# Optimization experiments

Measured on AMD Instinct MI355X. Metric: run time of the kernel, lower is better.

## Reference

```python
import jax, jax.numpy as jnp
import numpy as np

N = 20000   # nodes
E = 320000  # edges
C = 64      # channel multiplicity
NB = 8      # bessel basis size
NA = 4      # node attribute (species) dim
L_DIMS = (1, 3, 5)  # 2l+1 for l=0,1,2
SH = 9      # total spherical-harmonic dim
OFFS = (0, 1, 4, 9)


def setup_inputs() -> dict:
    key = jax.random.key(0)
    ks = jax.random.split(key, 11)
    s = lambda k, shape: jax.random.normal(k, shape, dtype=jnp.float32)
    return {
        "length": jax.random.uniform(ks[0], (E, NB), dtype=jnp.float32),
        "node_features": s(ks[1], (N, C)),
        "node_attributes": s(ks[2], (N, NA)),
        "edge_attributes": s(ks[3], (E, SH)),
        "W1": s(ks[4], (NB, 64)),
        "W2": s(ks[5], (64, 64)),
        "W3": s(ks[6], (64, 64)),
        "W4": s(ks[7], (64, 3 * C)),
        "Wl": s(ks[8], (3, C, C)),
        "Wsc": s(ks[9], (NA, C, C)),
        "edge_index": jax.random.randint(ks[10], (2, E), 0, N, dtype=jnp.int32),
    }


def reference(length, node_features, node_attributes, edge_attributes, W1, W2, W3, W4, Wl, Wsc, edge_index):
    sender, receiver = edge_index[0], edge_index[1]
    silu = jax.nn.silu
    # e3nn FullyConnectedNet: x @ W / sqrt(fan_in), silu between layers, no act on last
    h = silu(length @ W1 * np.float32(1.0 / np.sqrt(NB)))
    h = silu(h @ W2 * np.float32(0.125))
    h = silu(h @ W3 * np.float32(0.125))
    w = (h @ W4 * np.float32(0.125)).reshape(E, 3, C)  # per-edge TP weights [E,3,C]
    # weighted tensor product: scalar node feats x sh (0e x le -> le, uvu)
    wx = w * node_features[sender][:, None, :]          # [E,3,C]
    parts = []
    for l in range(3):
        Y = edge_attributes[:, OFFS[l]:OFFS[l + 1]]     # [E, 2l+1]
        parts.append((wx[:, l, :, None] * Y[:, None, :]).reshape(E, C * L_DIMS[l]))
    mij = jnp.concatenate(parts, axis=1)                # [E, C*9]
    # scatter_sum into receivers
    msg = jax.ops.segment_sum(mij, receiver, num_segments=N)  # [N, C*9]
    # e3nn Linear: per-l channel mix, 1/sqrt(fan_in) norm
    out_blocks = []
    o = 0
    for l in range(3):
        d = L_DIMS[l]
        blk = msg[:, o:o + C * d].reshape(N, C, d)
        out_blocks.append(jnp.einsum('num,uv->nvm', blk, Wl[l]) * np.float32(1.0 / np.sqrt(C)))
        o += C * d
    message = jnp.concatenate(out_blocks, axis=2)       # reshape_irreps -> [N, C, 9]
    # FullyConnectedTensorProduct(attr 0e, feat 0e) -> only 0e output has paths
    sc0 = jnp.einsum('na,nu,auw->nw', node_attributes, node_features, Wsc) * np.float32(1.0 / np.sqrt(NA * C))
    sc = jnp.concatenate([sc0, jnp.zeros((N, C * (SH - 1)), dtype=sc0.dtype)], axis=1)  # [N, C*9]
    return (message, sc)
```

## Files before the change

kernel.cpp:

```cpp
#include <hip/hip_runtime.h>
#include <hip/hip_fp16.h>

#define N_NODES 20000
#define N_EDGES 320000
#define MSG_ROW 576
#define MSG_OFF 11520000
#define SCAN_BS 256
#define NBLK_SCAN ((N_NODES + SCAN_BS - 1) / SCAN_BS)
#define NPAD 20032
#define MT_S (NPAD * 64)

typedef _Float16 f16;
typedef _Float16 f16x4 __attribute__((ext_vector_type(4)));
typedef _Float16 f16x8 __attribute__((ext_vector_type(8)));
typedef float f32x4 __attribute__((ext_vector_type(4)));

#define OFF_WT4 0
#define OFF_W1T 24576
#define OFF_WT2 28672
#define OFF_WT3 36864
#define WEDGE_BYTES 45056
#define OFF_H0  45056
#define OFF_HT  53248
#define LDS_TOTAL 69632
#define OFF_WXT 0

#define OFF_WLT  22528
#define OFF_WSCT 34816
#define WIMG_HALF 51200
#define WIMG_BYTES 102400

__device__ __forceinline__ float silu_f(float x) {
    return x * (1.0f / (1.0f + __expf(-x)));
}


__global__ __launch_bounds__(256)
void wimg_kernel(const float* __restrict__ W1, const float* __restrict__ W2,
                 const float* __restrict__ W3, const float* __restrict__ W4,
                 const float* __restrict__ Wl, const float* __restrict__ Wsc,
                 f16* __restrict__ img) {
    const int p = blockIdx.x * 256 + threadIdx.x;
    if (p >= WIMG_HALF) return;
    float v;
    if (p < 12288) {
        const int m = p >> 6, rem = p & 63, g = rem >> 3, j = rem & 7;
        const int k = ((g ^ (m & 7)) << 3) | j;
        v = W4[k * 192 + m];
    } else if (p < 14336) {
        const int q = p - 12288;
        const int m = q >> 5, rem = q & 31, g = rem >> 3, j = rem & 7;
        const int k = ((g ^ (m & 3)) << 3) | j;
        v = (k < 8) ? W1[k * 64 + m] : 0.f;
    } else if (p < 18432) {
        const int q = p - 14336;
        const int m = q >> 6, rem = q & 63, g = rem >> 3, j = rem & 7;
        const int k = ((g ^ (m & 7)) << 3) | j;
        v = W2[k * 64 + m];
    } else if (p < 22528) {
        const int q = p - 18432;
        const int m = q >> 6, rem = q & 63, g = rem >> 3, j = rem & 7;
        const int k = ((g ^ (m & 7)) << 3) | j;
        v = W3[k * 64 + m];
    } else if (p < OFF_WSCT) {
        const int q = p - OFF_WLT;
        const int l = q >> 12, r = q & 4095, vv = r >> 6, u = r & 63;
        v = Wl[(l * 64 + u) * 64 + vv];
    } else {
        const int q = p - OFF_WSCT;
        const int ww = q >> 8, kk = q & 255, a = kk >> 6, u = kk & 63;
        v = Wsc[(a * 64 + u) * 64 + ww];
    }
    img[p] = (f16)v;
}


__global__ __launch_bounds__(256)
void hist_kernel(const int* __restrict__ eidx, int* __restrict__ counts) {
    const int e = blockIdx.x * 256 + threadIdx.x;
    if (e < N_EDGES) atomicAdd(&counts[eidx[N_EDGES + e]], 1);
}

__global__ __launch_bounds__(SCAN_BS)
void scan1_kernel(const int* __restrict__ counts, int* __restrict__ offs,
                  int* __restrict__ bsum) {
    __shared__ int sm[SCAN_BS];
    const int tid = threadIdx.x;
    const int i = blockIdx.x * SCAN_BS + tid;
    const int v = (i < N_NODES) ? counts[i] : 0;
    sm[tid] = v;
    __syncthreads();
#pragma unroll
    for (int off = 1; off < SCAN_BS; off <<= 1) {
        const int t = (tid >= off) ? sm[tid - off] : 0;
        __syncthreads();
        sm[tid] += t;
        __syncthreads();
    }
    if (i < N_NODES) offs[i] = sm[tid] - v;
    if (tid == SCAN_BS - 1) bsum[blockIdx.x] = sm[tid];
}

__global__ __launch_bounds__(128)
void scan2_kernel(const int* __restrict__ bsum, int* __restrict__ bbase,
                  int* __restrict__ offs) {
    __shared__ int sm[128];
    const int tid = threadIdx.x;
    const int v = (tid < NBLK_SCAN) ? bsum[tid] : 0;
    sm[tid] = v;
    __syncthreads();
#pragma unroll
    for (int off = 1; off < 128; off <<= 1) {
        const int t = (tid >= off) ? sm[tid - off] : 0;
        __syncthreads();
        sm[tid] += t;
        __syncthreads();
    }
    if (tid < NBLK_SCAN) bbase[tid] = sm[tid] - v;
    if (tid == 127) offs[N_NODES] = sm[127];
}

__global__ __launch_bounds__(SCAN_BS)
void scan3_kernel(int* __restrict__ offs, const int* __restrict__ bbase,
                  int* __restrict__ cursor) {
    const int i = blockIdx.x * SCAN_BS + threadIdx.x;
    if (i < N_NODES) {
        const int o = offs[i] + bbase[blockIdx.x];
        offs[i] = o;
        cursor[i] = o;
    }
}

__global__ __launch_bounds__(256)
void scatter_kernel(const int* __restrict__ eidx, int* __restrict__ cursor,
                    int* __restrict__ order, int* __restrict__ rank) {
    const int e = blockIdx.x * 256 + threadIdx.x;
    if (e < N_EDGES) {
        const int pos = atomicAdd(&cursor[eidx[N_EDGES + e]], 1);
        order[pos] = e;
        rank[e] = pos;
    }
}


__global__ __launch_bounds__(512, 4)
void edge_mlp_mfma(const float* __restrict__ length,
                   const float* __restrict__ nf,
                   const int*   __restrict__ eidx,
                   const int*   __restrict__ rank,
                   const f16*   __restrict__ wimg,
                   f16* __restrict__ wx)
{
    __shared__ __align__(16) char s[LDS_TOTAL];
    __shared__ int sendS[128];
    __shared__ int rankS[128];

    const int tid = threadIdx.x;
    const int ebase = blockIdx.x << 7;

    {
        const uint4* src = (const uint4*)wimg;
        uint4* dst = (uint4*)s;
#pragma unroll
        for (int i = 0; i < 6; ++i) {
            const int c = i * 512 + tid;
            if (c < 2816) dst[c] = src[c];
        }
    }
    if (tid < 128) {
        const int e = tid;
        const float4 q0 = *(const float4*)&length[(size_t)(ebase + e) * 8];
        const float4 q1 = *(const float4*)&length[(size_t)(ebase + e) * 8 + 4];
        f16x8 h;
        h[0] = (f16)q0.x; h[1] = (f16)q0.y; h[2] = (f16)q0.z; h[3] = (f16)q0.w;
        h[4] = (f16)q1.x; h[5] = (f16)q1.y; h[6] = (f16)q1.z; h[7] = (f16)q1.w;
        *(f16x8*)(s + OFF_H0 + e * 64 + ((0 ^ (e & 3)) << 4)) = h;
        sendS[e] = eidx[ebase + e];
        rankS[e] = rank[ebase + e];
    } else {
        const int idx = tid - 128;
        const int e = idx / 3, gz = 1 + idx - (idx / 3) * 3;
        uint4 z; z.x = 0; z.y = 0; z.z = 0; z.w = 0;
        *(uint4*)(s + OFF_H0 + e * 64 + ((gz ^ (e & 3)) << 4)) = z;
    }
    __syncthreads();

    const int lane = tid & 63, w = tid >> 6;
    const int eh = w >> 2, wm = w & 3;
    const int lm = lane & 15, lg = lane >> 4;
    const int mrow = wm * 16 + lm;
    const int r0 = lg << 2;
    const int eloc0 = eh << 6;

    const f32x4 zacc = {0.f, 0.f, 0.f, 0.f};
    f32x4 acc[4];

    {
        const f16x8 a = *(const f16x8*)(s + OFF_W1T + mrow * 64 + ((lg ^ (mrow & 3)) << 4));
#pragma unroll
        for (int nt = 0; nt < 4; ++nt) {
            const int e = eloc0 + nt * 16 + lm;
            const f16x8 b = *(const f16x8*)(s + OFF_H0 + e * 64 + ((lg ^ (e & 3)) << 4));
            acc[nt] = __builtin_amdgcn_mfma_f32_16x16x32_f16(a, b, zacc, 0, 0, 0);
        }
    }
    {
        const int c = wm * 16 + r0;
#pragma unroll
        for (int nt = 0; nt < 4; ++nt) {
            const int e = eloc0 + nt * 16 + lm;
            f16x4 pk;
            pk[0] = (f16)silu_f(acc[nt][0] * 0.35355339059f);
            pk[1] = (f16)silu_f(acc[nt][1] * 0.35355339059f);
            pk[2] = (f16)silu_f(acc[nt][2] * 0.35355339059f);
            pk[3] = (f16)silu_f(acc[nt][3] * 0.35355339059f);
            *(f16x4*)(s + OFF_HT + e * 128 + (((c >> 3) ^ (e & 7)) << 4) + ((c & 7) << 1)) = pk;
        }
    }
    __syncthreads();

#pragma unroll
    for (int nt = 0; nt < 4; ++nt) acc[nt] = zacc;
#pragma unroll
    for (int kh = 0; kh < 2; ++kh) {
        const int g = (kh << 2) + lg;
        const f16x8 a = *(const f16x8*)(s + OFF_WT2 + mrow * 128 + ((g ^ (mrow & 7)) << 4));
#pragma unroll
        for (int nt = 0; nt < 4; ++nt) {
            const int e = eloc0 + nt * 16 + lm;
            const f16x8 b = *(const f16x8*)(s + OFF_HT + e * 128 + ((g ^ (e & 7)) << 4));
            acc[nt] = __builtin_amdgcn_mfma_f32_16x16x32_f16(a, b, acc[nt], 0, 0, 0);
        }
    }
    __syncthreads();
    {
        const int c = wm * 16 + r0;
#pragma unroll
        for (int nt = 0; nt < 4; ++nt) {
            const int e = eloc0 + nt * 16 + lm;
            f16x4 pk;
            pk[0] = (f16)silu_f(acc[nt][0] * 0.125f);
            pk[1] = (f16)silu_f(acc[nt][1] * 0.125f);
            pk[2] = (f16)silu_f(acc[nt][2] * 0.125f);
            pk[3] = (f16)silu_f(acc[nt][3] * 0.125f);
            *(f16x4*)(s + OFF_HT + e * 128 + (((c >> 3) ^ (e & 7)) << 4) + ((c & 7) << 1)) = pk;
        }
    }
    __syncthreads();

#pragma unroll
    for (int nt = 0; nt < 4; ++nt) acc[nt] = zacc;
#pragma unroll
    for (int kh = 0; kh < 2; ++kh) {
        const int g = (kh << 2) + lg;
        const f16x8 a = *(const f16x8*)(s + OFF_WT3 + mrow * 128 + ((g ^ (mrow & 7)) << 4));
#pragma unroll
        for (int nt = 0; nt < 4; ++nt) {
            const int e = eloc0 + nt * 16 + lm;
            const f16x8 b = *(const f16x8*)(s + OFF_HT + e * 128 + ((g ^ (e & 7)) << 4));
            acc[nt] = __builtin_amdgcn_mfma_f32_16x16x32_f16(a, b, acc[nt], 0, 0, 0);
        }
    }
    __syncthreads();
    {
        const int c = wm * 16 + r0;
#pragma unroll
        for (int nt = 0; nt < 4; ++nt) {
            const int e = eloc0 + nt * 16 + lm;
            f16x4 pk;
            pk[0] = (f16)silu_f(acc[nt][0] * 0.125f);
            pk[1] = (f16)silu_f(acc[nt][1] * 0.125f);
            pk[2] = (f16)silu_f(acc[nt][2] * 0.125f);
            pk[3] = (f16)silu_f(acc[nt][3] * 0.125f);
            *(f16x4*)(s + OFF_HT + e * 128 + (((c >> 3) ^ (e & 7)) << 4) + ((c & 7) << 1)) = pk;
        }
    }
    __syncthreads();

    f32x4 acc4[3][4];
#pragma unroll
    for (int p = 0; p < 3; ++p)
#pragma unroll
        for (int nt = 0; nt < 4; ++nt) acc4[p][nt] = zacc;
#pragma unroll
    for (int kh = 0; kh < 2; ++kh) {
        const int g = (kh << 2) + lg;
        f16x8 ap[3];
#pragma unroll
        for (int p = 0; p < 3; ++p) {
            const int m4 = p * 64 + mrow;
            ap[p] = *(const f16x8*)(s + OFF_WT4 + m4 * 128 + ((g ^ (m4 & 7)) << 4));
        }
#pragma unroll
        for (int nt = 0; nt < 4; ++nt) {
            const int e = eloc0 + nt * 16 + lm;
            const f16x8 b = *(const f16x8*)(s + OFF_HT + e * 128 + ((g ^ (e & 7)) << 4));
#pragma unroll
            for (int p = 0; p < 3; ++p)
                acc4[p][nt] = __builtin_amdgcn_mfma_f32_16x16x32_f16(ap[p], b, acc4[p][nt], 0, 0, 0);
        }
    }
    __syncthreads();

#pragma unroll
    for (int nt = 0; nt < 4; ++nt) {
        const int e = eloc0 + nt * 16 + lm;
        const int snd = sendS[e];
        const float4 nf4 = *(const float4*)&nf[(size_t)snd * 64 + wm * 16 + r0];
#pragma unroll
        for (int p = 0; p < 3; ++p) {
            const int c = p * 64 + wm * 16 + r0;
            f16x4 pk;
            pk[0] = (f16)(acc4[p][nt][0] * 0.125f * nf4.x);
            pk[1] = (f16)(acc4[p][nt][1] * 0.125f * nf4.y);
            pk[2] = (f16)(acc4[p][nt][2] * 0.125f * nf4.z);
            pk[3] = (f16)(acc4[p][nt][3] * 0.125f * nf4.w);
            *(f16x4*)(s + OFF_WXT + e * 384 + (((c >> 3) ^ (e & 7)) << 4) + ((c & 7) << 1)) = pk;
        }
    }
    __syncthreads();

#pragma unroll
    for (int it = 0; it < 6; ++it) {
        const int chunk = it * 512 + tid;
        const int e = chunk / 24, g = chunk - e * 24;
        const uint4 v = *(const uint4*)(s + OFF_WXT + e * 384 + ((g ^ (e & 7)) << 4));
        *(uint4*)((char*)wx + (size_t)rankS[e] * 384 + g * 16) = v;
    }
}


__global__ __launch_bounds__(256, 8)
void gather_kernel(const __half* __restrict__ wx,
                   const float* __restrict__ ea,
                   const int* __restrict__ offs,
                   const int* __restrict__ order,
                   f16* __restrict__ mT)
{
    const int tid = threadIdx.x;
    const int wid = tid >> 6;
    const int v   = tid & 63;
    const int n   = (blockIdx.x << 2) + wid;
    const int beg = offs[n];
    const int end = offs[n + 1];

    float a0 = 0.f, a1[3] = {0.f, 0.f, 0.f}, a2[5] = {0.f, 0.f, 0.f, 0.f, 0.f};
    int k = beg;
    for (; k + 2 <= end; k += 2) {
        const int eA = __builtin_amdgcn_readfirstlane(order[k]);
        const int eB = __builtin_amdgcn_readfirstlane(order[k + 1]);
        const __half* wrA = wx + (size_t)k * 192;
        const __half* wrB = wx + (size_t)(k + 1) * 192;
        const float xA0 = __half2float(wrA[v]);
        const float xA1 = __half2float(wrA[64 + v]);
        const float xA2 = __half2float(wrA[128 + v]);
        const float xB0 = __half2float(wrB[v]);
        const float xB1 = __half2float(wrB[64 + v]);
        const float xB2 = __half2float(wrB[128 + v]);
        const float* yA = ea + (size_t)eA * 9;
        const float* yB = ea + (size_t)eB * 9;
        a0 += xA0 * yA[0] + xB0 * yB[0];
#pragma unroll
        for (int m = 0; m < 3; ++m) a1[m] += xA1 * yA[1 + m] + xB1 * yB[1 + m];
#pragma unroll
        for (int m = 0; m < 5; ++m) a2[m] += xA2 * yA[4 + m] + xB2 * yB[4 + m];
    }
    if (k < end) {
        const int e = __builtin_amdgcn_readfirstlane(order[k]);
        const __half* wr = wx + (size_t)k * 192;
        const float x0 = __half2float(wr[v]);
        const float x1 = __half2float(wr[64 + v]);
        const float x2 = __half2float(wr[128 + v]);
        const float* y = ea + (size_t)e * 9;
        a0 += x0 * y[0];
#pragma unroll
        for (int m = 0; m < 3; ++m) a1[m] += x1 * y[1 + m];
#pragma unroll
        for (int m = 0; m < 5; ++m) a2[m] += x2 * y[4 + m];
    }

    f16* base = mT + (size_t)n * 64 + v;
    base[0] = (f16)a0;
#pragma unroll
    for (int m = 0; m < 3; ++m) base[(size_t)(1 + m) * MT_S] = (f16)a1[m];
#pragma unroll
    for (int m = 0; m < 5; ++m) base[(size_t)(4 + m) * MT_S] = (f16)a2[m];
}


__global__ __launch_bounds__(256, 2)
void node_mfma(const f16* __restrict__ wimg,
               const f16* __restrict__ mT,
               const float* __restrict__ nf,
               const float* __restrict__ na,
               float* __restrict__ out)
{
    __shared__ __align__(16) f16  mst[9 * 16 * 64];
    __shared__ __align__(16) f16  nft[16 * 64];
    __shared__ __align__(16) float nas[256];
    __shared__ __align__(16) float outb[16 * 580];

    const int tid = threadIdx.x;
    const int lane = tid & 63, w = tid >> 6;
    const int lm = lane & 15, lg = lane >> 4;
    const int r0 = lg << 2;
    const int n0 = blockIdx.x << 6;

    const f16* wlT  = wimg + OFF_WLT;
    const f16* wscT = wimg + OFF_WSCT;
    f16x8 wl[3][2];
#pragma unroll
    for (int l = 0; l < 3; ++l)
#pragma unroll
        for (int kk = 0; kk < 2; ++kk)
            wl[l][kk] = *(const f16x8*)(wlT + ((l << 6) + (w << 4) + lm) * 64 + (kk << 5) + (lg << 3));
    f16x8 wsc[8];
#pragma unroll
    for (int kg = 0; kg < 8; ++kg)
        wsc[kg] = *(const f16x8*)(wscT + ((w << 4) + lm) * 256 + (kg << 5) + (lg << 3));

    {
        const int n = n0 + (tid >> 2);
        nas[tid] = (n < N_NODES) ? na[(size_t)n * 4 + (tid & 3)] : 0.f;
    }

    const f32x4 zacc = {0.f, 0.f, 0.f, 0.f};

    for (int nt = 0; nt < 4; ++nt) {
        const int ng = n0 + (nt << 4);
        __syncthreads();

#pragma unroll
        for (int it = 0; it < 5; ++it) {
            const int c = it * 256 + tid;
            if (c < 1152) {
                const int m = c >> 7, rem = c & 127, r = rem >> 3, g = rem & 7;
                const uint4 v = *(const uint4*)(mT + (size_t)m * MT_S + (size_t)(ng + r) * 64 + (g << 3));
                *(uint4*)(&mst[m * 1024 + r * 64 + ((g ^ (r & 7)) << 3)]) = v;
            }
        }
        {
            const int r = tid >> 4, c4 = (tid & 15) << 2;
            const int n = ng + r;
            float4 v4;
            if (n < N_NODES) v4 = *(const float4*)&nf[(size_t)n * 64 + c4];
            else { v4.x = 0.f; v4.y = 0.f; v4.z = 0.f; v4.w = 0.f; }
            f16x4 h;
            h[0] = (f16)v4.x; h[1] = (f16)v4.y; h[2] = (f16)v4.z; h[3] = (f16)v4.w;
            const int g = c4 >> 3;
            *(f16x4*)&nft[r * 64 + ((g ^ (r & 7)) << 3) + (c4 & 7)] = h;
        }
        __syncthreads();

#pragma unroll
        for (int m = 0; m < 9; ++m) {
            const int l = (m == 0) ? 0 : ((m < 4) ? 1 : 2);
            f32x4 acc = zacc;
#pragma unroll
            for (int kk = 0; kk < 2; ++kk) {
                const int g = (kk << 2) + lg;
                const f16x8 b = *(const f16x8*)&mst[m * 1024 + lm * 64 + ((g ^ (lm & 7)) << 3)];
                acc = __builtin_amdgcn_mfma_f32_16x16x32_f16(wl[l][kk], b, acc, 0, 0, 0);
            }
#pragma unroll
            for (int i = 0; i < 4; ++i)
                outb[lm * 580 + ((w << 4) + r0 + i) * 9 + m] = acc[i] * 0.125f;
        }
        __syncthreads();

#pragma unroll
        for (int it = 0; it < 9; ++it) {
            const int c = it * 256 + tid;
            const int r = c / 144, q = c - r * 144;
            const int n = ng + r;
            if (n < N_NODES) {
                const float4 v = *(const float4*)&outb[r * 580 + (q << 2)];
                *(float4*)&out[(size_t)n * 576 + (q << 2)] = v;
            }
        }
        __syncthreads();

        {
            const float4 na4 = *(const float4*)&nas[((nt << 4) + lm) << 2];
            const float* nap = (const float*)&na4;
            f32x4 sacc = zacc;
#pragma unroll
            for (int kg = 0; kg < 8; ++kg) {
                const int g = ((kg & 1) << 2) + lg;
                f16x8 q = *(const f16x8*)&nft[lm * 64 + ((g ^ (lm & 7)) << 3)];
                const f16 sa = (f16)nap[kg >> 1];
                q = q * sa;
                sacc = __builtin_amdgcn_mfma_f32_16x16x32_f16(wsc[kg], q, sacc, 0, 0, 0);
            }
#pragma unroll
            for (int i = 0; i < 4; ++i)
                outb[lm * 580 + (w << 4) + r0 + i] = sacc[i] * 0.0625f;
        }
        __syncthreads();

        {
            const int r = tid >> 4, q = tid & 15;
            const int n = ng + r;
            if (n < N_NODES)
                *(float4*)&out[(size_t)MSG_OFF + (size_t)n * 576 + (q << 2)] =
                    *(const float4*)&outb[r * 580 + (q << 2)];
        }
        float4 z4; z4.x = 0.f; z4.y = 0.f; z4.z = 0.f; z4.w = 0.f;
#pragma unroll
        for (int it = 0; it < 8; ++it) {
            const int c = it * 256 + tid;
            const int r = c >> 7, q = c & 127;
            const int n = ng + r;
            if (n < N_NODES)
                *(float4*)&out[(size_t)MSG_OFF + (size_t)n * 576 + 64 + (q << 2)] = z4;
        }
    }
}


__device__ __forceinline__ void layer_accum(const float* src, const float* __restrict__ W,
                                            float a2[4][4], int c0, int e0) {
#pragma unroll
    for (int i = 0; i < 4; ++i)
#pragma unroll
        for (int j = 0; j < 4; ++j) a2[i][j] = 0.f;
#pragma unroll 8
    for (int u = 0; u < 64; ++u) {
        const float4 h4 = *(const float4*)&src[(u << 6) + e0];
        const float4 w4 = *(const float4*)&W[(u << 6) + c0];
        const float hv[4] = {h4.x, h4.y, h4.z, h4.w};
        const float wv[4] = {w4.x, w4.y, w4.z, w4.w};
#pragma unroll
        for (int i = 0; i < 4; ++i)
#pragma unroll
            for (int j = 0; j < 4; ++j) a2[i][j] += wv[i] * hv[j];
    }
}

__device__ __forceinline__ void layer_store(float* dst, const float a2[4][4],
                                            float scale, int c0, int e0) {
#pragma unroll
    for (int i = 0; i < 4; ++i) {
        float4 v;
        v.x = silu_f(a2[i][0] * scale);
        v.y = silu_f(a2[i][1] * scale);
        v.z = silu_f(a2[i][2] * scale);
        v.w = silu_f(a2[i][3] * scale);
        *(float4*)&dst[((c0 + i) << 6) + e0] = v;
    }
}

__global__ __launch_bounds__(256, 4)
void edge_kernel_atomic(const float* __restrict__ length,
                        const float* __restrict__ nf,
                        const float* __restrict__ ea,
                        const float* __restrict__ W1,
                        const float* __restrict__ W2,
                        const float* __restrict__ W3,
                        const float* __restrict__ W4,
                        const int*   __restrict__ eidx,
                        float* __restrict__ msg)
{
    __shared__ float buf[4096];
    __shared__ float lenS[512];
    __shared__ float Ys[576];
    __shared__ int   sendS[64];
    __shared__ int   recvS[64];

    const int tid = threadIdx.x;
    const int tx = tid & 15;
    const int ty = tid >> 4;
    const int c0 = tx << 2;
    const int e0 = ty << 2;
    const int ebase = blockIdx.x << 6;

    for (int i = tid; i < 512; i += 256) {
        const int e = i >> 3, k = i & 7;
        lenS[(k << 6) + e] = length[((ebase + e) << 3) + k];
    }
    for (int i = tid; i < 576; i += 256) Ys[i] = ea[ebase * 9 + i];
    if (tid < 64) {
        sendS[tid] = eidx[ebase + tid];
        recvS[tid] = eidx[N_EDGES + ebase + tid];
    }
    __syncthreads();

    {
        float a2[4][4];
#pragma unroll
        for (int i = 0; i < 4; ++i)
#pragma unroll
            for (int j = 0; j < 4; ++j) a2[i][j] = 0.f;
#pragma unroll
        for (int k = 0; k < 8; ++k) {
            const float4 h4 = *(const float4*)&lenS[(k << 6) + e0];
            const float4 w4 = *(const float4*)&W1[(k << 6) + c0];
            const float hv[4] = {h4.x, h4.y, h4.z, h4.w};
            const float wv[4] = {w4.x, w4.y, w4.z, w4.w};
#pragma unroll
            for (int i = 0; i < 4; ++i)
#pragma unroll
                for (int j = 0; j < 4; ++j) a2[i][j] += wv[i] * hv[j];
        }
        layer_store(buf, a2, 0.35355339059327373f, c0, e0);
    }
    __syncthreads();
    {
        float a2[4][4];
        layer_accum(buf, W2, a2, c0, e0);
        __syncthreads();
        layer_store(buf, a2, 0.125f, c0, e0);
    }
    __syncthreads();
    {
        float a2[4][4];
        layer_accum(buf, W3, a2, c0, e0);
        __syncthreads();
        layer_store(buf, a2, 0.125f, c0, e0);
    }
    __syncthreads();

    float wacc[3][4][4];
#pragma unroll
    for (int l = 0; l < 3; ++l)
#pragma unroll
        for (int i = 0; i < 4; ++i)
#pragma unroll
            for (int j = 0; j < 4; ++j) wacc[l][i][j] = 0.f;
#pragma unroll 4
    for (int u = 0; u < 64; ++u) {
        const float4 h4 = *(const float4*)&buf[(u << 6) + e0];
        const float hv[4] = {h4.x, h4.y, h4.z, h4.w};
#pragma unroll
        for (int l = 0; l < 3; ++l) {
            const float4 w4 = *(const float4*)&W4[u * 192 + (l << 6) + c0];
            const float wv[4] = {w4.x, w4.y, w4.z, w4.w};
#pragma unroll
            for (int i = 0; i < 4; ++i)
#pragma unroll
                for (int j = 0; j < 4; ++j) wacc[l][i][j] += wv[i] * hv[j];
        }
    }

#pragma unroll
    for (int j = 0; j < 4; ++j) {
        const int e = e0 + j;
        const int snd = sendS[e];
        const int rcv = recvS[e];
        const float4 nf4 = *(const float4*)&nf[(snd << 6) + c0];
        const float nfv[4] = {nf4.x, nf4.y, nf4.z, nf4.w};
        float* mrow = msg + rcv * MSG_ROW;
        const float y0 = Ys[e * 9 + 0];
        float y1[3], y2[5];
#pragma unroll
        for (int m = 0; m < 3; ++m) y1[m] = Ys[e * 9 + 1 + m];
#pragma unroll
        for (int m = 0; m < 5; ++m) y2[m] = Ys[e * 9 + 4 + m];
#pragma unroll
        for (int i = 0; i < 4; ++i) {
            const int c = c0 + i;
            const float wx0 = wacc[0][i][j] * 0.125f * nfv[i];
            const float wx1 = wacc[1][i][j] * 0.125f * nfv[i];
            const float wx2 = wacc[2][i][j] * 0.125f * nfv[i];
            atomicAdd(&mrow[c], wx0 * y0);
#pragma unroll
            for (int m = 0; m < 3; ++m) atomicAdd(&mrow[64 + c * 3 + m], wx1 * y1[m]);
#pragma unroll
            for (int m = 0; m < 5; ++m) atomicAdd(&mrow[256 + c * 5 + m], wx2 * y2[m]);
        }
    }
}

__global__ __launch_bounds__(256, 4)
void node_kernel(const float* __restrict__ nf,
                 const float* __restrict__ na,
                 const float* __restrict__ Wl,
                 const float* __restrict__ Wsc,
                 float* __restrict__ out)
{
    __shared__ float ms[4][576];
    __shared__ float fs[4][64];
    const int tid = threadIdx.x;
    const int wid = tid >> 6;
    const int v   = tid & 63;
    const int n   = (blockIdx.x << 2) + wid;
    const float* msg = out + MSG_OFF;

#pragma unroll
    for (int j = 0; j < 9; ++j)
        ms[wid][(j << 6) + v] = msg[n * MSG_ROW + (j << 6) + v];
    fs[wid][v] = nf[(n << 6) + v];
    __syncthreads();

    float o9[9];
#pragma unroll
    for (int j = 0; j < 9; ++j) o9[j] = 0.f;
    const float* m0 = &ms[wid][0];
    const float* m1 = &ms[wid][64];
    const float* m2 = &ms[wid][256];

#pragma unroll 8
    for (int u = 0; u < 64; ++u) {
        const float w0 = Wl[(u << 6) + v];
        const float w1 = Wl[4096 + (u << 6) + v];
        const float w2 = Wl[8192 + (u << 6) + v];
        o9[0] += m0[u] * w0;
        o9[1] += m1[u * 3 + 0] * w1;
        o9[2] += m1[u * 3 + 1] * w1;
        o9[3] += m1[u * 3 + 2] * w1;
        o9[4] += m2[u * 5 + 0] * w2;
        o9[5] += m2[u * 5 + 1] * w2;
        o9[6] += m2[u * 5 + 2] * w2;
        o9[7] += m2[u * 5 + 3] * w2;
        o9[8] += m2[u * 5 + 4] * w2;
    }
#pragma unroll
    for (int j = 0; j < 9; ++j) out[n * MSG_ROW + v * 9 + j] = o9[j] * 0.125f;

    const float b0 = na[(n << 2) + 0];
    const float b1 = na[(n << 2) + 1];
    const float b2 = na[(n << 2) + 2];
    const float b3 = na[(n << 2) + 3];
    float sacc = 0.f;
#pragma unroll 8
    for (int u = 0; u < 64; ++u) {
        const float f = fs[wid][u];
        sacc += f * (b0 * Wsc[(u << 6) + v] + b1 * Wsc[4096 + (u << 6) + v] +
                     b2 * Wsc[8192 + (u << 6) + v] + b3 * Wsc[12288 + (u << 6) + v]);
    }
    float* scrow = out + MSG_OFF + n * MSG_ROW;
    scrow[v] = sacc * 0.0625f;
#pragma unroll
    for (int j = 1; j < 9; ++j) scrow[(j << 6) + v] = 0.f;
}

extern "C" void kernel_launch(void* const* d_in, const int* in_sizes, int n_in,
                              void* d_out, int out_size, void* d_ws, size_t ws_size,
                              hipStream_t stream) {
    const float* length = (const float*)d_in[0];
    const float* nfeat  = (const float*)d_in[1];
    const float* nattr  = (const float*)d_in[2];
    const float* eattr  = (const float*)d_in[3];
    const float* W1     = (const float*)d_in[4];
    const float* W2     = (const float*)d_in[5];
    const float* W3     = (const float*)d_in[6];
    const float* W4     = (const float*)d_in[7];
    const float* Wl     = (const float*)d_in[8];
    const float* Wsc    = (const float*)d_in[9];
    const int*   eidx   = (const int*)d_in[10];
    float* out = (float*)d_out;

    f16*    wimg   = (f16*)d_ws;
    __half* wx     = (__half*)((char*)d_ws + WIMG_BYTES);
    f16*    mT     = (f16*)((char*)d_ws + WIMG_BYTES + (size_t)N_EDGES * 192 * 2);
    int*   counts  = (int*)((char*)mT + (size_t)9 * MT_S * 2);
    int*   offsets = counts + N_NODES;
    int*   cursor  = offsets + N_NODES + 1;
    int*   order   = cursor + N_NODES;
    int*   rank    = order + N_EDGES;
    int*   bsum    = rank + N_EDGES;
    int*   bbase   = bsum + 128;
    const size_t need = WIMG_BYTES + (size_t)N_EDGES * 192 * 2 + (size_t)9 * MT_S * 2 +
                        (size_t)(N_NODES * 3 + 1 + N_EDGES * 2 + 256) * 4;

    if (ws_size >= need) {
        hipMemsetAsync(counts, 0, N_NODES * sizeof(int), stream);
        wimg_kernel<<<(WIMG_HALF + 255) / 256, 256, 0, stream>>>(W1, W2, W3, W4, Wl, Wsc, wimg);
        hist_kernel<<<N_EDGES / 256, 256, 0, stream>>>(eidx, counts);
        scan1_kernel<<<NBLK_SCAN, SCAN_BS, 0, stream>>>(counts, offsets, bsum);
        scan2_kernel<<<1, 128, 0, stream>>>(bsum, bbase, offsets);
        scan3_kernel<<<NBLK_SCAN, SCAN_BS, 0, stream>>>(offsets, bbase, cursor);
        scatter_kernel<<<N_EDGES / 256, 256, 0, stream>>>(eidx, cursor, order, rank);
        edge_mlp_mfma<<<N_EDGES / 128, 512, 0, stream>>>(length, nfeat, eidx, rank,
                                                         wimg, (f16*)wx);
        gather_kernel<<<N_NODES / 4, 256, 0, stream>>>(wx, eattr, offsets, order, mT);
        node_mfma<<<NPAD / 64, 256, 0, stream>>>(wimg, mT, nfeat, nattr, out);
    } else {
        hipMemsetAsync(out + MSG_OFF, 0, (size_t)N_NODES * MSG_ROW * sizeof(float), stream);
        edge_kernel_atomic<<<N_EDGES / 64, 256, 0, stream>>>(length, nfeat, eattr,
                                                             W1, W2, W3, W4, eidx,
                                                             out + MSG_OFF);
        node_kernel<<<N_NODES / 4, 256, 0, stream>>>(nfeat, nattr, Wl, Wsc, out);
    }
}
```

Measured before the change: 165.6 us.

## Fuse gather into node MFMA kernel and merge weight-image with histogram

After: 223.8 us. +35.1%, slower.

```diff
diff --git a/kernel.cpp b/kernel.cpp
--- a/kernel.cpp
+++ b/kernel.cpp
@@ -8,7 +8,6 @@
 #define SCAN_BS 256
 #define NBLK_SCAN ((N_NODES + SCAN_BS - 1) / SCAN_BS)
 #define NPAD 20032
-#define MT_S (NPAD * 64)
 
 typedef _Float16 f16;
 typedef _Float16 f16x4 __attribute__((ext_vector_type(4)));
@@ -19,7 +18,6 @@
 #define OFF_W1T 24576
 #define OFF_WT2 28672
 #define OFF_WT3 36864
-#define WEDGE_BYTES 45056
 #define OFF_H0  45056
 #define OFF_HT  53248
 #define LDS_TOTAL 69632
@@ -29,6 +27,7 @@
 #define OFF_WSCT 34816
 #define WIMG_HALF 51200
 #define WIMG_BYTES 102400
+#define WIMG_BLOCKS 200
 
 __device__ __forceinline__ float silu_f(float x) {
     return x * (1.0f / (1.0f + __expf(-x)));
@@ -36,12 +35,18 @@
 
 
 __global__ __launch_bounds__(256)
-void wimg_kernel(const float* __restrict__ W1, const float* __restrict__ W2,
-                 const float* __restrict__ W3, const float* __restrict__ W4,
-                 const float* __restrict__ Wl, const float* __restrict__ Wsc,
-                 f16* __restrict__ img) {
-    const int p = blockIdx.x * 256 + threadIdx.x;
-    if (p >= WIMG_HALF) return;
+void pre_kernel(const float* __restrict__ W1, const float* __restrict__ W2,
+                const float* __restrict__ W3, const float* __restrict__ W4,
+                const float* __restrict__ Wl, const float* __restrict__ Wsc,
+                f16* __restrict__ img,
+                const int* __restrict__ eidx, int* __restrict__ counts) {
+    const int b = blockIdx.x;
+    if (b >= WIMG_BLOCKS) {
+        const int e = (b - WIMG_BLOCKS) * 256 + threadIdx.x;
+        if (e < N_EDGES) atomicAdd(&counts[eidx[N_EDGES + e]], 1);
+        return;
+    }
+    const int p = b * 256 + threadIdx.x;
     float v;
     if (p < 12288) {
         const int m = p >> 6, rem = p & 63, g = rem >> 3, j = rem & 7;
@@ -75,12 +80,6 @@
 }
 
 
-__global__ __launch_bounds__(256)
-void hist_kernel(const int* __restrict__ eidx, int* __restrict__ counts) {
-    const int e = blockIdx.x * 256 + threadIdx.x;
-    if (e < N_EDGES) atomicAdd(&counts[eidx[N_EDGES + e]], 1);
-}
-
 __global__ __launch_bounds__(SCAN_BS)
 void scan1_kernel(const int* __restrict__ counts, int* __restrict__ offs,
                   int* __restrict__ bsum) {
@@ -330,70 +329,15 @@
 }
 
 
-__global__ __launch_bounds__(256, 8)
-void gather_kernel(const __half* __restrict__ wx,
-                   const float* __restrict__ ea,
-                   const int* __restrict__ offs,
-                   const int* __restrict__ order,
-                   f16* __restrict__ mT)
-{
-    const int tid = threadIdx.x;
-    const int wid = tid >> 6;
-    const int v   = tid & 63;
-    const int n   = (blockIdx.x << 2) + wid;
-    const int beg = offs[n];
-    const int end = offs[n + 1];
-
-    float a0 = 0.f, a1[3] = {0.f, 0.f, 0.f}, a2[5] = {0.f, 0.f, 0.f, 0.f, 0.f};
-    int k = beg;
-    for (; k + 2 <= end; k += 2) {
-        const int eA = __builtin_amdgcn_readfirstlane(order[k]);
-        const int eB = __builtin_amdgcn_readfirstlane(order[k + 1]);
-        const __half* wrA = wx + (size_t)k * 192;
-        const __half* wrB = wx + (size_t)(k + 1) * 192;
-        const float xA0 = __half2float(wrA[v]);
-        const float xA1 = __half2float(wrA[64 + v]);
-        const float xA2 = __half2float(wrA[128 + v]);
-        const float xB0 = __half2float(wrB[v]);
-        const float xB1 = __half2float(wrB[64 + v]);
-        const float xB2 = __half2float(wrB[128 + v]);
-        const float* yA = ea + (size_t)eA * 9;
-        const float* yB = ea + (size_t)eB * 9;
-        a0 += xA0 * yA[0] + xB0 * yB[0];
-#pragma unroll
-        for (int m = 0; m < 3; ++m) a1[m] += xA1 * yA[1 + m] + xB1 * yB[1 + m];
-#pragma unroll
-        for (int m = 0; m < 5; ++m) a2[m] += xA2 * yA[4 + m] + xB2 * yB[4 + m];
-    }
-    if (k < end) {
-        const int e = __builtin_amdgcn_readfirstlane(order[k]);
-        const __half* wr = wx + (size_t)k * 192;
-        const float x0 = __half2float(wr[v]);
-        const float x1 = __half2float(wr[64 + v]);
-        const float x2 = __half2float(wr[128 + v]);
-        const float* y = ea + (size_t)e * 9;
-        a0 += x0 * y[0];
-#pragma unroll
-        for (int m = 0; m < 3; ++m) a1[m] += x1 * y[1 + m];
-#pragma unroll
-        for (int m = 0; m < 5; ++m) a2[m] += x2 * y[4 + m];
-    }
-
-    f16* base = mT + (size_t)n * 64 + v;
-    base[0] = (f16)a0;
-#pragma unroll
-    for (int m = 0; m < 3; ++m) base[(size_t)(1 + m) * MT_S] = (f16)a1[m];
-#pragma unroll
-    for (int m = 0; m < 5; ++m) base[(size_t)(4 + m) * MT_S] = (f16)a2[m];
-}
-
-
 __global__ __launch_bounds__(256, 2)
-void node_mfma(const f16* __restrict__ wimg,
-               const f16* __restrict__ mT,
-               const float* __restrict__ nf,
-               const float* __restrict__ na,
-               float* __restrict__ out)
+void gather_node_mfma(const __half* __restrict__ wx,
+                      const float* __restrict__ ea,
+                      const int* __restrict__ offs,
+                      const int* __restrict__ order,
+                      const f16* __restrict__ wimg,
+                      const float* __restrict__ nf,
+                      const float* __restrict__ na,
+                      float* __restrict__ out)
 {
     __shared__ __align__(16) f16  mst[9 * 16 * 64];
     __shared__ __align__(16) f16  nft[16 * 64];
@@ -430,15 +374,58 @@
         const int ng = n0 + (nt << 4);
         __syncthreads();
 
-#pragma unroll
-        for (int it = 0; it < 5; ++it) {
-            const int c = it * 256 + tid;
-            if (c < 1152) {
-                const int m = c >> 7, rem = c & 127, r = rem >> 3, g = rem & 7;
-                const uint4 v = *(const uint4*)(mT + (size_t)m * MT_S + (size_t)(ng + r) * 64 + (g << 3));
-                *(uint4*)(&mst[m * 1024 + r * 64 + ((g ^ (r & 7)) << 3)]) = v;
+        const int swz = (((lane >> 3) ^ 0) << 3) + (lane & 7);
+#pragma unroll
+        for (int j = 0; j < 4; ++j) {
+            const int r = (w << 2) + j;
+            const int n = ng + r;
+            float a0 = 0.f, a1[3] = {0.f, 0.f, 0.f}, a2[5] = {0.f, 0.f, 0.f, 0.f, 0.f};
+            if (n < N_NODES) {
+                const int beg = offs[n];
+                const int end = offs[n + 1];
+                int k = beg;
+                for (; k + 2 <= end; k += 2) {
+                    const int eA = __builtin_amdgcn_readfirstlane(order[k]);
+                    const int eB = __builtin_amdgcn_readfirstlane(order[k + 1]);
+                    const __half* wrA = wx + (size_t)k * 192;
+                    const __half* wrB = wx + (size_t)(k + 1) * 192;
+                    const float xA0 = __half2float(wrA[lane]);
+                    const float xA1 = __half2float(wrA[64 + lane]);
+                    const float xA2 = __half2float(wrA[128 + lane]);
+                    const float xB0 = __half2float(wrB[lane]);
+                    const float xB1 = __half2float(wrB[64 + lane]);
+                    const float xB2 = __half2float(wrB[128 + lane]);
+                    const float* yA = ea + (size_t)eA * 9;
+                    const float* yB = ea + (size_t)eB * 9;
+                    a0 += xA0 * yA[0] + xB0 * yB[0];
+#pragma unroll
+                    for (int m = 0; m < 3; ++m) a1[m] += xA1 * yA[1 + m] + xB1 * yB[1 + m];
+#pragma unroll
+                    for (int m = 0; m < 5; ++m) a2[m] += xA2 * yA[4 + m] + xB2 * yB[4 + m];
+                }
+                if (k < end) {
+                    const int e = __builtin_amdgcn_readfirstlane(order[k]);
+                    const __half* wr = wx + (size_t)k * 192;
+                    const float x0 = __half2float(wr[lane]);
+                    const float x1 = __half2float(wr[64 + lane]);
+                    const float x2 = __half2float(wr[128 + lane]);
+                    const float* y = ea + (size_t)e * 9;
+                    a0 += x0 * y[0];
+#pragma unroll
+                    for (int m = 0; m < 3; ++m) a1[m] += x1 * y[1 + m];
+#pragma unroll
+                    for (int m = 0; m < 5; ++m) a2[m] += x2 * y[4 + m];
+                }
             }
-        }
+            const int sw = r * 64 + ((((lane >> 3) ^ (r & 7))) << 3) + (lane & 7);
+            mst[sw] = (f16)a0;
+#pragma unroll
+            for (int m = 0; m < 3; ++m) mst[(1 + m) * 1024 + sw] = (f16)a1[m];
+#pragma unroll
+            for (int m = 0; m < 5; ++m) mst[(4 + m) * 1024 + sw] = (f16)a2[m];
+        }
+        (void)swz;
+
         {
             const int r = tid >> 4, c4 = (tid & 15) << 2;
             const int n = ng + r;
@@ -752,29 +739,28 @@
 
     f16*    wimg   = (f16*)d_ws;
     __half* wx     = (__half*)((char*)d_ws + WIMG_BYTES);
-    f16*    mT     = (f16*)((char*)d_ws + WIMG_BYTES + (size_t)N_EDGES * 192 * 2);
-    int*   counts  = (int*)((char*)mT + (size_t)9 * MT_S * 2);
+    int*   counts  = (int*)((char*)d_ws + WIMG_BYTES + (size_t)N_EDGES * 192 * 2);
     int*   offsets = counts + N_NODES;
     int*   cursor  = offsets + N_NODES + 1;
     int*   order   = cursor + N_NODES;
     int*   rank    = order + N_EDGES;
     int*   bsum    = rank + N_EDGES;
     int*   bbase   = bsum + 128;
-    const size_t need = WIMG_BYTES + (size_t)N_EDGES * 192 * 2 + (size_t)9 * MT_S * 2 +
+    const size_t need = WIMG_BYTES + (size_t)N_EDGES * 192 * 2 +
                         (size_t)(N_NODES * 3 + 1 + N_EDGES * 2 + 256) * 4;
 
     if (ws_size >= need) {
         hipMemsetAsync(counts, 0, N_NODES * sizeof(int), stream);
-        wimg_kernel<<<(WIMG_HALF + 255) / 256, 256, 0, stream>>>(W1, W2, W3, W4, Wl, Wsc, wimg);
-        hist_kernel<<<N_EDGES / 256, 256, 0, stream>>>(eidx, counts);
+        pre_kernel<<<WIMG_BLOCKS + N_EDGES / 256, 256, 0, stream>>>(W1, W2, W3, W4, Wl, Wsc,
+                                                                    wimg, eidx, counts);
         scan1_kernel<<<NBLK_SCAN, SCAN_BS, 0, stream>>>(counts, offsets, bsum);
         scan2_kernel<<<1, 128, 0, stream>>>(bsum, bbase, offsets);
         scan3_kernel<<<NBLK_SCAN, SCAN_BS, 0, stream>>>(offsets, bbase, cursor);
         scatter_kernel<<<N_EDGES / 256, 256, 0, stream>>>(eidx, cursor, order, rank);
         edge_mlp_mfma<<<N_EDGES / 128, 512, 0, stream>>>(length, nfeat, eidx, rank,
                                                          wimg, (f16*)wx);
-        gather_kernel<<<N_NODES / 4, 256, 0, stream>>>(wx, eattr, offsets, order, mT);
-        node_mfma<<<NPAD / 64, 256, 0, stream>>>(wimg, mT, nfeat, nattr, out);
+        gather_node_mfma<<<NPAD / 64, 256, 0, stream>>>(wx, eattr, offsets, order,
+                                                        wimg, nfeat, nattr, out);
     } else {
         hipMemsetAsync(out + MSG_OFF, 0, (size_t)N_NODES * MSG_ROW * sizeof(float), stream);
         edge_kernel_atomic<<<N_EDGES / 64, 256, 0, stream>>>(length, nfeat, eattr,
```

## Fuse preprocessing kernels to cut launch count in CSR build

Applied to the files above, without the earlier changes.

New measurement: 150.5 us. 1.1x faster.

```diff
diff --git a/kernel.cpp b/kernel.cpp
--- a/kernel.cpp
+++ b/kernel.cpp
@@ -19,7 +19,6 @@
 #define OFF_W1T 24576
 #define OFF_WT2 28672
 #define OFF_WT3 36864
-#define WEDGE_BYTES 45056
 #define OFF_H0  45056
 #define OFF_HT  53248
 #define LDS_TOTAL 69632
@@ -29,6 +28,7 @@
 #define OFF_WSCT 34816
 #define WIMG_HALF 51200
 #define WIMG_BYTES 102400
+#define WIMG_BLOCKS 200
 
 __device__ __forceinline__ float silu_f(float x) {
     return x * (1.0f / (1.0f + __expf(-x)));
@@ -36,12 +36,18 @@
 
 
 __global__ __launch_bounds__(256)
-void wimg_kernel(const float* __restrict__ W1, const float* __restrict__ W2,
-                 const float* __restrict__ W3, const float* __restrict__ W4,
-                 const float* __restrict__ Wl, const float* __restrict__ Wsc,
-                 f16* __restrict__ img) {
-    const int p = blockIdx.x * 256 + threadIdx.x;
-    if (p >= WIMG_HALF) return;
+void pre_kernel(const float* __restrict__ W1, const float* __restrict__ W2,
+                const float* __restrict__ W3, const float* __restrict__ W4,
+                const float* __restrict__ Wl, const float* __restrict__ Wsc,
+                f16* __restrict__ img,
+                const int* __restrict__ eidx, int* __restrict__ counts) {
+    const int b = blockIdx.x;
+    if (b >= WIMG_BLOCKS) {
+        const int e = (b - WIMG_BLOCKS) * 256 + threadIdx.x;
+        if (e < N_EDGES) atomicAdd(&counts[eidx[N_EDGES + e]], 1);
+        return;
+    }
+    const int p = b * 256 + threadIdx.x;
     float v;
     if (p < 12288) {
         const int m = p >> 6, rem = p & 63, g = rem >> 3, j = rem & 7;
@@ -75,12 +81,6 @@
 }
 
 
-__global__ __launch_bounds__(256)
-void hist_kernel(const int* __restrict__ eidx, int* __restrict__ counts) {
-    const int e = blockIdx.x * 256 + threadIdx.x;
-    if (e < N_EDGES) atomicAdd(&counts[eidx[N_EDGES + e]], 1);
-}
-
 __global__ __launch_bounds__(SCAN_BS)
 void scan1_kernel(const int* __restrict__ counts, int* __restrict__ offs,
                   int* __restrict__ bsum) {
@@ -101,45 +101,23 @@
     if (tid == SCAN_BS - 1) bsum[blockIdx.x] = sm[tid];
 }
 
-__global__ __launch_bounds__(128)
-void scan2_kernel(const int* __restrict__ bsum, int* __restrict__ bbase,
-                  int* __restrict__ offs) {
-    __shared__ int sm[128];
+__global__ __launch_bounds__(SCAN_BS)
+void scan3_kernel(int* __restrict__ offs, const int* __restrict__ bsum,
+                  int* __restrict__ cursor) {
+    __shared__ int bs[NBLK_SCAN];
     const int tid = threadIdx.x;
-    const int v = (tid < NBLK_SCAN) ? bsum[tid] : 0;
-    sm[tid] = v;
-    __syncthreads();
-#pragma unroll
-    for (int off = 1; off < 128; off <<= 1) {
-        const int t = (tid >= off) ? sm[tid - off] : 0;
-        __syncthreads();
-        sm[tid] += t;
-        __syncthreads();
-    }
-    if (tid < NBLK_SCAN) bbase[tid] = sm[tid] - v;
-    if (tid == 127) offs[N_NODES] = sm[127];
-}
-
-__global__ __launch_bounds__(SCAN_BS)
-void scan3_kernel(int* __restrict__ offs, const int* __restrict__ bbase,
-                  int* __restrict__ cursor) {
-    const int i = blockIdx.x * SCAN_BS + threadIdx.x;
+    if (tid < NBLK_SCAN) bs[tid] = bsum[tid];
+    __syncthreads();
+    int bbase = 0;
+    for (int j = 0; j < blockIdx.x; ++j) bbase += bs[j];
+    const int i = blockIdx.x * SCAN_BS + tid;
     if (i < N_NODES) {
-        const int o = offs[i] + bbase[blockIdx.x];
+        const int o = offs[i] + bbase;
         offs[i] = o;
         cursor[i] = o;
     }
-}
-
-__global__ __launch_bounds__(256)
-void scatter_kernel(const int* __restrict__ eidx, int* __restrict__ cursor,
-                    int* __restrict__ order, int* __restrict__ rank) {
-    const int e = blockIdx.x * 256 + threadIdx.x;
-    if (e < N_EDGES) {
-        const int pos = atomicAdd(&cursor[eidx[N_EDGES + e]], 1);
-        order[pos] = e;
-        rank[e] = pos;
-    }
+    if (blockIdx.x == NBLK_SCAN - 1 && tid == SCAN_BS - 1)
+        offs[N_NODES] = bbase + bs[NBLK_SCAN - 1];
 }
 
 
@@ -147,7 +125,8 @@
 void edge_mlp_mfma(const float* __restrict__ length,
                    const float* __restrict__ nf,
                    const int*   __restrict__ eidx,
-                   const int*   __restrict__ rank,
+                   int* __restrict__ cursor,
+                   int* __restrict__ order,
                    const f16*   __restrict__ wimg,
                    f16* __restrict__ wx)
 {
@@ -169,14 +148,18 @@
     }
     if (tid < 128) {
         const int e = tid;
-        const float4 q0 = *(const float4*)&length[(size_t)(ebase + e) * 8];
-        const float4 q1 = *(const float4*)&length[(size_t)(ebase + e) * 8 + 4];
+        const int eg = ebase + e;
+        const float4 q0 = *(const float4*)&length[(size_t)eg * 8];
+        const float4 q1 = *(const float4*)&length[(size_t)eg * 8 + 4];
         f16x8 h;
         h[0] = (f16)q0.x; h[1] = (f16)q0.y; h[2] = (f16)q0.z; h[3] = (f16)q0.w;
         h[4] = (f16)q1.x; h[5] = (f16)q1.y; h[6] = (f16)q1.z; h[7] = (f16)q1.w;
         *(f16x8*)(s + OFF_H0 + e * 64 + ((0 ^ (e & 3)) << 4)) = h;
-        sendS[e] = eidx[ebase + e];
-        rankS[e] = rank[ebase + e];
+        sendS[e] = eidx[eg];
+        const int rcv = eidx[N_EDGES + eg];
+        const int pos = atomicAdd(&cursor[rcv], 1);
+        order[pos] = eg;
+        rankS[e] = pos;
     } else {
         const int idx = tid - 128;
         const int e = idx / 3, gz = 1 + idx - (idx / 3) * 3;
@@ -757,21 +740,17 @@
     int*   offsets = counts + N_NODES;
     int*   cursor  = offsets + N_NODES + 1;
     int*   order   = cursor + N_NODES;
-    int*   rank    = order + N_EDGES;
-    int*   bsum    = rank + N_EDGES;
-    int*   bbase   = bsum + 128;
+    int*   bsum    = order + N_EDGES;
     const size_t need = WIMG_BYTES + (size_t)N_EDGES * 192 * 2 + (size_t)9 * MT_S * 2 +
-                        (size_t)(N_NODES * 3 + 1 + N_EDGES * 2 + 256) * 4;
+                        (size_t)(N_NODES * 3 + 1 + N_EDGES + 128) * 4;
 
     if (ws_size >= need) {
         hipMemsetAsync(counts, 0, N_NODES * sizeof(int), stream);
-        wimg_kernel<<<(WIMG_HALF + 255) / 256, 256, 0, stream>>>(W1, W2, W3, W4, Wl, Wsc, wimg);
-        hist_kernel<<<N_EDGES / 256, 256, 0, stream>>>(eidx, counts);
+        pre_kernel<<<WIMG_BLOCKS + N_EDGES / 256, 256, 0, stream>>>(W1, W2, W3, W4, Wl, Wsc,
+                                                                    wimg, eidx, counts);
         scan1_kernel<<<NBLK_SCAN, SCAN_BS, 0, stream>>>(counts, offsets, bsum);
-        scan2_kernel<<<1, 128, 0, stream>>>(bsum, bbase, offsets);
-        scan3_kernel<<<NBLK_SCAN, SCAN_BS, 0, stream>>>(offsets, bbase, cursor);
-        scatter_kernel<<<N_EDGES / 256, 256, 0, stream>>>(eidx, cursor, order, rank);
-        edge_mlp_mfma<<<N_EDGES / 128, 512, 0, stream>>>(length, nfeat, eidx, rank,
+        scan3_kernel<<<NBLK_SCAN, SCAN_BS, 0, stream>>>(offsets, bsum, cursor);
+        edge_mlp_mfma<<<N_EDGES / 128, 512, 0, stream>>>(length, nfeat, eidx, cursor, order,
                                                          wimg, (f16*)wx);
         gather_kernel<<<N_NODES / 4, 256, 0, stream>>>(wx, eattr, offsets, order, mT);
         node_mfma<<<NPAD / 64, 256, 0, stream>>>(wimg, mT, nfeat, nattr, out);
```
